# Optimization experiments

Measured on AMD Instinct MI355X. Metric: run time of the kernel, lower is better.

The kernel has to match this reference:

```python
import jax, jax.numpy as jnp
import numpy as np

NUM_BINS = 10
BIN_DISP = 0.5
MIN_REG = 1e-5
H = 22
W = 22
S = 16
C = 256
F_ = H * W


def _distance_map(center, sz):
    # DiMP DistanceMap: soft-binned radial distance from center. [bins, sz0, sz1]
    bins = jnp.arange(NUM_BINS, dtype=jnp.float32)[:, None, None]
    k0 = jnp.arange(sz[0], dtype=jnp.float32)[:, None]
    k1 = jnp.arange(sz[1], dtype=jnp.float32)[None, :]
    dist = jnp.sqrt((k0 - center[0]) ** 2 + (k1 - center[1]) ** 2)
    bd = dist[None] / BIN_DISP - bins
    lower = jax.nn.relu(1.0 - jnp.abs(bd[:-1]))
    last = jnp.clip(1.0 + bd[-1:], 0.0, 1.0)
    return jnp.concatenate([lower, last], axis=0)


def _unfold_map(fm, h, w):
    # Equivalent of F.unfold(full_map,(h,w)).view(h,w,h,w).flip((2,3)).permute(2,3,0,1):
    # out[f=(li,lj), ki, kj] = fm[h-1-li+ki, w-1-lj+kj]
    r = (h - 1 - jnp.arange(h))[:, None] + jnp.arange(h)[None, :]  # [li, ki]
    c = (w - 1 - jnp.arange(w))[:, None] + jnp.arange(w)[None, :]  # [lj, kj]
    m = fm[r[:, None, :, None], c[None, :, None, :]]  # [li, lj, ki, kj]
    return m.reshape(h * w, h, w)


def setup_inputs() -> dict:
    key = jax.random.key(0)
    k1, k2 = jax.random.split(key)
    filt = jax.random.normal(k1, (S, F_, C, 1, 1), jnp.float32) * 0.1
    feat = jax.random.normal(k2, (1, S, C, H, W), jnp.float32)
    d = jnp.arange(NUM_BINS, dtype=jnp.float32) * BIN_DISP
    init_gauss = jnp.exp(-0.5 * d ** 2)  # init_gauss_sigma = 1.0
    return {
        "filt": filt,
        "feat": feat,
        "log_step_length": jnp.zeros((1,), jnp.float32),          # log(1.0)
        "filter_reg": 0.01 * jnp.ones((1,), jnp.float32),
        "label_w": init_gauss - init_gauss.min(),                  # label_map_predictor weights
        "mask_w": 4.0 * jnp.tanh(2.0 - d),                         # target_mask_predictor weights
        "spatial_w": jnp.ones((NUM_BINS,), jnp.float32),           # spatial_weight_predictor weights
        "num_iter": 3,
    }


def _forward(filt, feat, log_step_length, filter_reg, label_w, mask_w, spatial_w, num_iter):
    f2 = feat[0]            # [S, C, H, W]
    w = filt[..., 0, 0]     # [S, F, C]   (1x1 DiCor filters)
    h, wd = feat.shape[-2], feat.shape[-1]
    s, fnum = w.shape[0], w.shape[1]
    sz = (2 * h - 1, 2 * wd - 1)
    center = jnp.array([sz[0] // 2, sz[1] // 2], dtype=jnp.float32)
    dmap = _distance_map(center, sz)  # [bins, 2H-1, 2W-1]
    # 1x1 convs over the bin dimension, then unfold into per-filter maps [F, H, W]
    label_map = _unfold_map(jnp.einsum('bhw,b->hw', dmap, label_w), h, wd)
    target_mask = _unfold_map(jax.nn.sigmoid(jnp.einsum('bhw,b->hw', dmap, mask_w)), h, wd)
    spatial_weight = _unfold_map(jnp.einsum('bhw,b->hw', dmap, spatial_w), h, wd)
    step_length = jnp.exp(log_step_length[0])
    reg_weight = jnp.maximum(filter_reg[0] * filter_reg[0], MIN_REG ** 2)
    a = target_mask
    sw2 = spatial_weight * spatial_weight
    for _ in range(num_iter):
        # apply_filter with 1x1 filters: scores[s,f,h,w] = sum_c feat[s,c,h,w] * w[s,f,c]
        scores = jnp.einsum('schw,sfc->sfhw', f2, w)
        # LeakyReluPar / LeakyReluParDeriv with per-location slope a
        scores_act = 0.5 * (1.0 - a) * jnp.abs(scores) + 0.5 * (1.0 + a) * scores
        score_mask = 0.5 * (1.0 - a) * jnp.sign(scores) + 0.5 * (1.0 + a)
        residuals = score_mask * (sw2 * (scores_act - label_map))
        # apply_feat_transpose with 1x1 filters
        w_grad = jnp.einsum('sfhw,schw->sfc', residuals, f2) + reg_weight * w
        scores_grad = jnp.einsum('schw,sfc->sfhw', f2, w_grad)
        scores_grad = spatial_weight * (score_mask * scores_grad)
        alpha_num = jnp.sum(w_grad * w_grad, axis=2)  # [S, F]
        alpha_den = jnp.maximum(
            jnp.sum((scores_grad * scores_grad).reshape(s, fnum, -1), axis=2)
            + reg_weight * alpha_num, 1e-8)
        alpha = alpha_num / alpha_den
        w = w - step_length * alpha[..., None] * w_grad
    return w[..., None, None]  # [S, F, C, 1, 1]


def reference(filt, feat, log_step_length, filter_reg, label_w, mask_w, spatial_w, num_iter):
    return _forward(filt, feat, log_step_length, filter_reg, label_w, mask_w, spatial_w, num_iter)
```

## Files before the change

kernel.cpp:

```cpp
#include <hip/hip_runtime.h>
#include <math.h>
#include <stdint.h>

#define Ww 22
#define P_ 484
#define S_ 16
#define C_ 256
#define TSZ 1849

typedef _Float16 f16x8 __attribute__((ext_vector_type(8)));
typedef _Float16 f16x4 __attribute__((ext_vector_type(4)));
typedef float f32x4 __attribute__((ext_vector_type(4)));

__device__ __forceinline__ int xcd_chunk(int bid, int chunk) {
    return (bid & 7) * chunk + (bid >> 3);
}

__device__ __forceinline__ void gld16(const _Float16* g, _Float16* lds) {
    auto* lp = (__attribute__((address_space(3))) uint32_t*)(uintptr_t)(lds);
    auto* gp = (const __attribute__((address_space(1))) uint32_t*)(uintptr_t)(g);
    __builtin_amdgcn_global_load_lds(gp, lp, 16, 0, 0);
}

__device__ __forceinline__ f32x4 map_entry(const float* label_w, const float* mask_w,
                                           const float* spatial_w, float d) {
    float lab = 0.f, msk = 0.f, spw = 0.f;
#pragma unroll
    for (int b = 0; b < 9; ++b) {
        float wb = fmaxf(0.f, 1.f - fabsf(d - (float)b));
        lab += wb * label_w[b];
        msk += wb * mask_w[b];
        spw += wb * spatial_w[b];
    }
    float w9 = fminf(fmaxf(1.f + (d - 9.f), 0.f), 1.f);
    lab += w9 * label_w[9];
    msk += w9 * mask_w[9];
    spw += w9 * spatial_w[9];
    f32x4 o;
    o[0] = lab;
    o[1] = 1.f / (1.f + expf(-msk));
    o[2] = spw * spw;
    o[3] = spw;
    return o;
}

__global__ __launch_bounds__(256) void k_pro(
    const float* __restrict__ filt, const float* __restrict__ feat,
    const float* __restrict__ lw, const float* __restrict__ mw,
    const float* __restrict__ sw,
    float* __restrict__ Wf, _Float16* __restrict__ Wh,
    float* __restrict__ num0, float* __restrict__ den0,
    _Float16* __restrict__ f2h, _Float16* __restrict__ f2th,
    f32x4* __restrict__ map4t) {
    int wgid = xcd_chunk(blockIdx.x, 514);
    int x = wgid / 514;
    int local = wgid % 514;
    int t = threadIdx.x;
    if (local == 0) {
        int idx = x + 8 * t;
        if (idx < TSZ) {
            int dx = idx / 43 - 21, dy = idx % 43 - 21;
            float d = sqrtf((float)(dx * dx + dy * dy)) * 2.0f;
            map4t[idx] = map_entry(lw, mw, sw, d);
        }
    } else if (local < 257) {
        int u = local - 1;
        int s = x * 2 + (u >> 7);
        int f = (u & 127) * 4 + (t >> 6);
        int c = (t & 63) * 4;
        size_t oh = ((size_t)(s * 512 + f)) * C_ + c;
        if (f < P_) {
            size_t o = ((size_t)(s * P_ + f)) * C_ + c;
            f32x4 v = *(const f32x4*)(filt + o);
            *(f32x4*)(Wf + o) = v;
            f16x4 h;
#pragma unroll
            for (int q = 0; q < 4; ++q) h[q] = (_Float16)v[q];
            *(f16x4*)(Wh + oh) = h;
            if ((t & 63) == 0) { num0[s * P_ + f] = 0.f; den0[s * P_ + f] = 0.f; }
        } else {
            f16x4 h = {};
            *(f16x4*)(Wh + oh) = h;
        }
    } else if (local < 513) {
        int u = local - 257;
        int s = x * 2 + (u >> 7);
        int rem = u & 127;
        int p0 = (rem & 15) * 32, c0 = (rem >> 4) * 32;
        int cc = t & 31, rr = t >> 5;
        __shared__ float tb[32][33];
#pragma unroll
        for (int q = 0; q < 4; ++q) {
            int c = c0 + rr + q * 8;
            int p = p0 + cc;
            float v = (p < P_) ? feat[((size_t)s * C_ + c) * P_ + p] : 0.f;
            f2h[((size_t)s * C_ + c) * 512 + p] = (_Float16)v;
            tb[rr + q * 8][cc] = v;
        }
        __syncthreads();
#pragma unroll
        for (int q = 0; q < 4; ++q) {
            int p = p0 + rr + q * 8;
            f2th[((size_t)s * 512 + p) * C_ + c0 + cc] = (_Float16)tb[cc][rr + q * 8];
        }
    }
}

template <int EPI, int BM, int KK, int LDA, int LDB, int TPS, int NBN, bool WSG = false>
__global__ __launch_bounds__(256, 4) void k_gemm(
    const _Float16* __restrict__ Ah, const _Float16* __restrict__ Bh,
    const f32x4* __restrict__ map4t, const _Float16* __restrict__ sch_i,
    const _Float16* __restrict__ Wh_i, const float* __restrict__ freg,
    _Float16* __restrict__ out_h, _Float16* __restrict__ out_h3,
    float* __restrict__ red) {
    constexpr int TI = BM / 32, TJ = 2, NT = KK / 128, NIA = BM / 16;
    int tid = threadIdx.x;
    int w = tid >> 6, l = tid & 63;
    int wgid = xcd_chunk(blockIdx.x, S_ * TPS / 8);
    int s = wgid / TPS;
    int rem = wgid % TPS;
    int m0 = (rem / NBN) * BM, n0 = (rem % NBN) * 64;
    int wm = w >> 1, wn = w & 1;
    int r16 = l & 15;

    __shared__ _Float16 As[BM * 128];
    __shared__ _Float16 Bs[64 * 128];

    int lrow = w * 4 + (l >> 4);
    int gsrc = ((l & 15) ^ lrow) << 3;
    const _Float16* gA = Ah + (size_t)s * (512 * LDA) + (size_t)(m0 + lrow) * LDA + gsrc;
    const _Float16* gB = Bh + (size_t)s * 131072 + (size_t)(n0 + lrow) * LDB + gsrc;

    f32x4 acc[TI][TJ] = {};

#pragma unroll
    for (int t = 0; t < NT; ++t) {
#pragma unroll
        for (int i = 0; i < NIA; ++i)
            gld16(gA + (size_t)i * 16 * LDA + t * 128, &As[(i * 16 + w * 4) * 128]);
#pragma unroll
        for (int i = 0; i < 4; ++i)
            gld16(gB + (size_t)i * 16 * LDB + t * 128, &Bs[(i * 16 + w * 4) * 128]);
        __syncthreads();
#pragma unroll
        for (int kk = 0; kk < 4; ++kk) {
            int px = ((kk * 4 + (l >> 4)) ^ r16) << 3;
            f16x8 af[TI], bf[TJ];
#pragma unroll
            for (int ti = 0; ti < TI; ++ti)
                af[ti] = *(const f16x8*)&As[(wm * (BM / 2) + ti * 16 + r16) * 128 + px];
#pragma unroll
            for (int tj = 0; tj < TJ; ++tj)
                bf[tj] = *(const f16x8*)&Bs[(wn * 32 + tj * 16 + r16) * 128 + px];
#pragma unroll
            for (int ti = 0; ti < TI; ++ti)
#pragma unroll
                for (int tj = 0; tj < TJ; ++tj)
                    acc[ti][tj] = __builtin_amdgcn_mfma_f32_16x16x32_f16(
                        af[ti], bf[tj], acc[ti][tj], 0, 0, 0);
        }
        if (t + 1 < NT) __syncthreads();
    }

    int q4 = (l >> 4) * 4;

    if constexpr (EPI == 1) {
#pragma unroll
        for (int ti = 0; ti < TI; ++ti)
#pragma unroll
            for (int r = 0; r < 4; ++r) {
                int m = m0 + wm * (BM / 2) + ti * 16 + q4 + r;
                int im = m / 22, jm = m - im * 22;
#pragma unroll
                for (int tj = 0; tj < TJ; ++tj) {
                    int n = n0 + wn * 32 + tj * 16 + r16;
                    float sc = acc[ti][tj][r];
                    float res = 0.f;
                    size_t po = ((size_t)(s * 512 + m)) * 512 + n;
                    if (m < P_ && n < P_) {
                        int kn = n / 22, ln = n - kn * 22;
                        f32x4 m4 = map4t[(kn - im + 21) * 43 + (ln - jm + 21)];
                        float sgn = (sc > 0.f) ? 1.f : ((sc < 0.f) ? -1.f : 0.f);
                        float msk = 0.5f * (1.f - m4[1]) * sgn + 0.5f * (1.f + m4[1]);
                        res = msk * (m4[2] * (msk * sc - m4[0]));
                    }
                    out_h[po] = (_Float16)res;
                    out_h3[po] = (_Float16)sc;
                }
            }
    } else if constexpr (EPI == 2) {
        float fr = freg[0];
        float regw = fmaxf(fr * fr, 1e-10f);
#pragma unroll
        for (int ti = 0; ti < TI; ++ti)
#pragma unroll
            for (int r = 0; r < 4; ++r) {
                int m = m0 + wm * (BM / 2) + ti * 16 + q4 + r;
                float v = 0.f;
#pragma unroll
                for (int tj = 0; tj < TJ; ++tj) {
                    int n = n0 + wn * 32 + tj * 16 + r16;
                    size_t o = ((size_t)(s * 512 + m)) * C_ + n;
                    float wg = acc[ti][tj][r] + regw * (float)Wh_i[o];
                    out_h[o] = (_Float16)wg;
                    v += wg * wg;
                }
                v += __shfl_xor(v, 1);
                v += __shfl_xor(v, 2);
                v += __shfl_xor(v, 4);
                v += __shfl_xor(v, 8);
                if (r16 == 0 && m < P_) atomicAdd(&red[s * P_ + m], v);
            }
    } else {
#pragma unroll
        for (int ti = 0; ti < TI; ++ti)
#pragma unroll
            for (int r = 0; r < 4; ++r) {
                int m = m0 + wm * (BM / 2) + ti * 16 + q4 + r;
                int im = m / 22, jm = m - im * 22;
                float v = 0.f;
#pragma unroll
                for (int tj = 0; tj < TJ; ++tj) {
                    int n = n0 + wn * 32 + tj * 16 + r16;
                    float a = acc[ti][tj][r];
                    size_t po = ((size_t)(s * 512 + m)) * 512 + n;
                    if constexpr (WSG) out_h[po] = (_Float16)a;
                    if (m < P_ && n < P_) {
                        int kn = n / 22, ln = n - kn * 22;
                        f32x4 m4 = map4t[(kn - im + 21) * 43 + (ln - jm + 21)];
                        float sc = (float)sch_i[po];
                        float sgn = (sc > 0.f) ? 1.f : ((sc < 0.f) ? -1.f : 0.f);
                        float msk = 0.5f * (1.f - m4[1]) * sgn + 0.5f * (1.f + m4[1]);
                        float sg = m4[3] * msk * a;
                        v += sg * sg;
                    }
                }
                v += __shfl_xor(v, 1);
                v += __shfl_xor(v, 2);
                v += __shfl_xor(v, 4);
                v += __shfl_xor(v, 8);
                if (r16 == 0 && m < P_) atomicAdd(&red[s * P_ + m], v);
            }
    }
}

__global__ __launch_bounds__(256) void k_fu(
    float* __restrict__ Wf, _Float16* __restrict__ Wh,
    const _Float16* __restrict__ wgradh,
    const float* __restrict__ num_rd, const float* __restrict__ den_rd,
    float* __restrict__ num_zw, float* __restrict__ den_zw,
    const _Float16* __restrict__ sgrawh, _Float16* __restrict__ scoresh,
    _Float16* __restrict__ residh,
    const f32x4* __restrict__ map4t,
    const float* __restrict__ freg, const float* __restrict__ lsl) {
    int wgid = xcd_chunk(blockIdx.x, 484);
    int s = wgid / 242;
    int local = wgid % 242;
    int t = threadIdx.x;
    float fr = freg[0];
    float regw = fmaxf(fr * fr, 1e-10f);
    float step = expf(lsl[0]);
    if (local < 121) {
        int f = local * 4 + (t >> 6);
        int row = s * P_ + f;
        float nu = num_rd[row], de = den_rd[row];
        float sa = step * (nu / fmaxf(de + regw * nu, 1e-8f));
        int c = (t & 63) * 4;
        size_t o = (size_t)row * C_ + c;
        size_t oh = ((size_t)(s * 512 + f)) * C_ + c;
        f32x4 wv = *(const f32x4*)(Wf + o);
        f16x4 g = *(const f16x4*)(wgradh + oh);
        f16x4 h;
#pragma unroll
        for (int q = 0; q < 4; ++q) {
            wv[q] -= sa * (float)g[q];
            h[q] = (_Float16)wv[q];
        }
        *(f32x4*)(Wf + o) = wv;
        *(f16x4*)(Wh + oh) = h;
        if ((t & 63) == 0) { num_zw[row] = 0.f; den_zw[row] = 0.f; }
    } else {
        int m = (local - 121) * 4 + (t >> 6);
        int row = s * P_ + m;
        float nu = num_rd[row], de = den_rd[row];
        float sa = step * (nu / fmaxf(de + regw * nu, 1e-8f));
        int im = m / 22, jm = m - im * 22;
        int n0 = (t & 63) * 8;
        size_t ro = ((size_t)(s * 512 + m)) * 512 + n0;
        f16x8 so = *(const f16x8*)(scoresh + ro);
        f16x8 gg = *(const f16x8*)(sgrawh + ro);
        f16x8 sn, rs;
#pragma unroll
        for (int j = 0; j < 8; ++j) {
            float sc = (float)so[j] - sa * (float)gg[j];
            sn[j] = (_Float16)sc;
            int n = n0 + j;
            float res = 0.f;
            if (n < P_) {
                int kn = n / 22, ln = n - kn * 22;
                f32x4 m4 = map4t[(kn - im + 21) * 43 + (ln - jm + 21)];
                float sgn = (sc > 0.f) ? 1.f : ((sc < 0.f) ? -1.f : 0.f);
                float msk = 0.5f * (1.f - m4[1]) * sgn + 0.5f * (1.f + m4[1]);
                res = msk * (m4[2] * (msk * sc - m4[0]));
            }
            rs[j] = (_Float16)res;
        }
        *(f16x8*)(scoresh + ro) = sn;
        *(f16x8*)(residh + ro) = rs;
    }
}

__global__ __launch_bounds__(256) void k_update(float* __restrict__ Wf,
                                                const _Float16* __restrict__ wgradh,
                                                const float* __restrict__ num,
                                                const float* __restrict__ den,
                                                const float* __restrict__ freg,
                                                const float* __restrict__ lsl) {
    int wgid = xcd_chunk(blockIdx.x, 242);
    int s = wgid / 121;
    int t = threadIdx.x;
    int f = (wgid % 121) * 4 + (t >> 6);
    int row = s * P_ + f;
    float nu = num[row], de = den[row];
    float fr = freg[0];
    float regw = fmaxf(fr * fr, 1e-10f);
    float sa = expf(lsl[0]) * (nu / fmaxf(de + regw * nu, 1e-8f));
    int c = (t & 63) * 4;
    size_t o = (size_t)row * C_ + c;
    size_t oh = ((size_t)(s * 512 + f)) * C_ + c;
    f32x4 wv = *(const f32x4*)(Wf + o);
    f16x4 g = *(const f16x4*)(wgradh + oh);
#pragma unroll
    for (int q = 0; q < 4; ++q) wv[q] -= sa * (float)g[q];
    *(f32x4*)(Wf + o) = wv;
}

extern "C" void kernel_launch(void* const* d_in, const int* in_sizes, int n_in,
                              void* d_out, int out_size, void* d_ws, size_t ws_size,
                              hipStream_t stream) {
    const float* filt = (const float*)d_in[0];
    const float* feat = (const float*)d_in[1];
    const float* lsl  = (const float*)d_in[2];
    const float* freg = (const float*)d_in[3];
    const float* lw   = (const float*)d_in[4];
    const float* mw   = (const float*)d_in[5];
    const float* sw   = (const float*)d_in[6];
    float* Wf = (float*)d_out;

    char* ws = (char*)d_ws;
    f32x4* map4t     = (f32x4*)ws;      ws += (size_t)TSZ * 16;
    _Float16* residh = (_Float16*)ws;   ws += (size_t)S_ * 512 * 512 * 2;
    _Float16* scoresh= (_Float16*)ws;   ws += (size_t)S_ * 512 * 512 * 2;
    _Float16* sgrawh = (_Float16*)ws;   ws += (size_t)S_ * 512 * 512 * 2;
    _Float16* wgradh = (_Float16*)ws;   ws += (size_t)S_ * 512 * C_ * 2;
    _Float16* Wh     = (_Float16*)ws;   ws += (size_t)S_ * 512 * C_ * 2;
    _Float16* f2h    = (_Float16*)ws;   ws += (size_t)S_ * C_ * 512 * 2;
    _Float16* f2th   = (_Float16*)ws;   ws += (size_t)S_ * 512 * C_ * 2;
    float* num0      = (float*)ws;      ws += (size_t)S_ * P_ * 4;
    float* den0      = (float*)ws;      ws += (size_t)S_ * P_ * 4;
    float* num1      = (float*)ws;      ws += (size_t)S_ * P_ * 4;
    float* den1      = (float*)ws;      ws += (size_t)S_ * P_ * 4;

    k_pro<<<4112, 256, 0, stream>>>(filt, feat, lw, mw, sw, Wf, Wh, num0, den0,
                                    f2h, f2th, map4t);

    k_gemm<1, 64, 256, 256, 256, 64, 8><<<1024, 256, 0, stream>>>(
        Wh, f2th, map4t, nullptr, nullptr, nullptr, residh, scoresh, nullptr);
    k_gemm<2, 32, 512, 512, 512, 64, 4><<<1024, 256, 0, stream>>>(
        residh, f2h, map4t, nullptr, Wh, freg, wgradh, nullptr, num0);
    k_gemm<3, 64, 256, 256, 256, 64, 8, true><<<1024, 256, 0, stream>>>(
        wgradh, f2th, map4t, scoresh, nullptr, nullptr, sgrawh, nullptr, den0);
    k_fu<<<3872, 256, 0, stream>>>(Wf, Wh, wgradh, num0, den0, num1, den1,
                                   sgrawh, scoresh, residh, map4t, freg, lsl);
    k_gemm<2, 32, 512, 512, 512, 64, 4><<<1024, 256, 0, stream>>>(
        residh, f2h, map4t, nullptr, Wh, freg, wgradh, nullptr, num1);
    k_gemm<3, 64, 256, 256, 256, 64, 8, true><<<1024, 256, 0, stream>>>(
        wgradh, f2th, map4t, scoresh, nullptr, nullptr, sgrawh, nullptr, den1);
    k_fu<<<3872, 256, 0, stream>>>(Wf, Wh, wgradh, num1, den1, num0, den0,
                                   sgrawh, scoresh, residh, map4t, freg, lsl);
    k_gemm<2, 32, 512, 512, 512, 64, 4><<<1024, 256, 0, stream>>>(
        residh, f2h, map4t, nullptr, Wh, freg, wgradh, nullptr, num0);
    k_gemm<3, 64, 256, 256, 256, 64, 8, false><<<1024, 256, 0, stream>>>(
        wgradh, f2th, map4t, scoresh, nullptr, nullptr, nullptr, nullptr, den0);
    k_update<<<1936, 256, 0, stream>>>(Wf, wgradh, num0, den0, freg, lsl);
}
```

Before: 128.5 us.

## Fuse filter/score update elementwise pass into the residual-by-features gemm

Replaces the separate elementwise update kernel and the following wgrad gemm with one kernel. It computes the updated scores and residuals on the fly into LDS as the A operand, multiplies them by the features, and then applies the filter step and regularisation in the epilogue. Scores are ping-ponged between two buffers, and six zeroed num/den accumulators are set up once in the prologue so later kernels no longer re-zero them. This removes a kernel launch and the residual round-trip through global memory per iteration. In exchange the residual and score math is recomputed in each of the four N-tile blocks, and the tile is small (32x64, K staged in 128-wide chunks without double buffering).

```diff
diff --git a/kernel.cpp b/kernel.cpp
--- a/kernel.cpp
+++ b/kernel.cpp
@@ -7,6 +7,7 @@
 #define S_ 16
 #define C_ 256
 #define TSZ 1849
+#define NB 7744
 
 typedef _Float16 f16x8 __attribute__((ext_vector_type(8)));
 typedef _Float16 f16x4 __attribute__((ext_vector_type(4)));
@@ -49,7 +50,7 @@
     const float* __restrict__ lw, const float* __restrict__ mw,
     const float* __restrict__ sw,
     float* __restrict__ Wf, _Float16* __restrict__ Wh,
-    float* __restrict__ num0, float* __restrict__ den0,
+    float* __restrict__ nb,
     _Float16* __restrict__ f2h, _Float16* __restrict__ f2th,
     f32x4* __restrict__ map4t) {
     int wgid = xcd_chunk(blockIdx.x, 514);
@@ -77,7 +78,11 @@
 #pragma unroll
             for (int q = 0; q < 4; ++q) h[q] = (_Float16)v[q];
             *(f16x4*)(Wh + oh) = h;
-            if ((t & 63) == 0) { num0[s * P_ + f] = 0.f; den0[s * P_ + f] = 0.f; }
+            if ((t & 63) == 0) {
+                int row = s * P_ + f;
+#pragma unroll
+                for (int b = 0; b < 6; ++b) nb[b * NB + row] = 0.f;
+            }
         } else {
             f16x4 h = {};
             *(f16x4*)(Wh + oh) = h;
@@ -244,69 +249,132 @@
     }
 }
 
-__global__ __launch_bounds__(256) void k_fu(
+__global__ __launch_bounds__(256, 4) void k_g2f(
+    const _Float16* __restrict__ sch_old, _Float16* __restrict__ sch_new,
+    const _Float16* __restrict__ sgrawh, const _Float16* __restrict__ Bh,
     float* __restrict__ Wf, _Float16* __restrict__ Wh,
-    const _Float16* __restrict__ wgradh,
+    _Float16* __restrict__ wgradh,
     const float* __restrict__ num_rd, const float* __restrict__ den_rd,
-    float* __restrict__ num_zw, float* __restrict__ den_zw,
-    const _Float16* __restrict__ sgrawh, _Float16* __restrict__ scoresh,
-    _Float16* __restrict__ residh,
+    float* __restrict__ num_wr,
     const f32x4* __restrict__ map4t,
     const float* __restrict__ freg, const float* __restrict__ lsl) {
-    int wgid = xcd_chunk(blockIdx.x, 484);
-    int s = wgid / 242;
-    int local = wgid % 242;
-    int t = threadIdx.x;
+    __shared__ _Float16 As[32 * 128];
+    __shared__ _Float16 Bs[64 * 128];
+    __shared__ float alpha_l[32];
+
+    int tid = threadIdx.x;
+    int w = tid >> 6, l = tid & 63;
+    int wgid = xcd_chunk(blockIdx.x, 128);
+    int s = wgid / 64;
+    int rem = wgid % 64;
+    int m0 = (rem >> 2) * 32, n0 = (rem & 3) * 64;
+    int wm = w >> 1, wn = w & 1;
+    int r16 = l & 15;
+
     float fr = freg[0];
     float regw = fmaxf(fr * fr, 1e-10f);
     float step = expf(lsl[0]);
-    if (local < 121) {
-        int f = local * 4 + (t >> 6);
-        int row = s * P_ + f;
-        float nu = num_rd[row], de = den_rd[row];
-        float sa = step * (nu / fmaxf(de + regw * nu, 1e-8f));
-        int c = (t & 63) * 4;
-        size_t o = (size_t)row * C_ + c;
-        size_t oh = ((size_t)(s * 512 + f)) * C_ + c;
-        f32x4 wv = *(const f32x4*)(Wf + o);
-        f16x4 g = *(const f16x4*)(wgradh + oh);
-        f16x4 h;
-#pragma unroll
-        for (int q = 0; q < 4; ++q) {
-            wv[q] -= sa * (float)g[q];
-            h[q] = (_Float16)wv[q];
-        }
-        *(f32x4*)(Wf + o) = wv;
-        *(f16x4*)(Wh + oh) = h;
-        if ((t & 63) == 0) { num_zw[row] = 0.f; den_zw[row] = 0.f; }
-    } else {
-        int m = (local - 121) * 4 + (t >> 6);
-        int row = s * P_ + m;
-        float nu = num_rd[row], de = den_rd[row];
-        float sa = step * (nu / fmaxf(de + regw * nu, 1e-8f));
-        int im = m / 22, jm = m - im * 22;
-        int n0 = (t & 63) * 8;
-        size_t ro = ((size_t)(s * 512 + m)) * 512 + n0;
-        f16x8 so = *(const f16x8*)(scoresh + ro);
-        f16x8 gg = *(const f16x8*)(sgrawh + ro);
-        f16x8 sn, rs;
-#pragma unroll
-        for (int j = 0; j < 8; ++j) {
-            float sc = (float)so[j] - sa * (float)gg[j];
-            sn[j] = (_Float16)sc;
-            int n = n0 + j;
-            float res = 0.f;
-            if (n < P_) {
-                int kn = n / 22, ln = n - kn * 22;
-                f32x4 m4 = map4t[(kn - im + 21) * 43 + (ln - jm + 21)];
-                float sgn = (sc > 0.f) ? 1.f : ((sc < 0.f) ? -1.f : 0.f);
-                float msk = 0.5f * (1.f - m4[1]) * sgn + 0.5f * (1.f + m4[1]);
-                res = msk * (m4[2] * (msk * sc - m4[0]));
-            }
-            rs[j] = (_Float16)res;
-        }
-        *(f16x8*)(scoresh + ro) = sn;
-        *(f16x8*)(residh + ro) = rs;
+
+    if (tid < 32) {
+        int mg = m0 + tid;
+        float a = 0.f;
+        if (mg < P_) {
+            int row = s * P_ + mg;
+            float nu = num_rd[row], de = den_rd[row];
+            a = step * (nu / fmaxf(de + regw * nu, 1e-8f));
+        }
+        alpha_l[tid] = a;
+    }
+    __syncthreads();
+
+    int lrow = w * 4 + (l >> 4);
+    int gsrc = ((l & 15) ^ lrow) << 3;
+    const _Float16* gB = Bh + (size_t)s * 131072 + (size_t)(n0 + lrow) * 512 + gsrc;
+
+    f32x4 acc[2] = {};
+    bool wr_sc = (n0 == 0);
+    size_t sbase = ((size_t)(s * 512 + m0)) * 512;
+
+#pragma unroll
+    for (int t = 0; t < 4; ++t) {
+#pragma unroll
+        for (int i = 0; i < 4; ++i)
+            gld16(gB + (size_t)i * 16 * 512 + t * 128, &Bs[(i * 16 + w * 4) * 128]);
+#pragma unroll
+        for (int i = 0; i < 2; ++i) {
+            int gidx = tid + i * 256;
+            int row = gidx >> 4, g = gidx & 15;
+            int mg = m0 + row;
+            int im = mg / 22, jm = mg - im * 22;
+            size_t ro = sbase + (size_t)row * 512 + t * 128 + g * 8;
+            f16x8 so = *(const f16x8*)(sch_old + ro);
+            f16x8 sg = *(const f16x8*)(sgrawh + ro);
+            float sa = alpha_l[row];
+            f16x8 sn, rs;
+#pragma unroll
+            for (int j = 0; j < 8; ++j) {
+                float sc = (float)so[j] - sa * (float)sg[j];
+                sn[j] = (_Float16)sc;
+                int n = t * 128 + g * 8 + j;
+                float res = 0.f;
+                if (mg < P_ && n < P_) {
+                    int kn = n / 22, ln = n - kn * 22;
+                    f32x4 m4 = map4t[(kn - im + 21) * 43 + (ln - jm + 21)];
+                    float sgn = (sc > 0.f) ? 1.f : ((sc < 0.f) ? -1.f : 0.f);
+                    float msk = 0.5f * (1.f - m4[1]) * sgn + 0.5f * (1.f + m4[1]);
+                    res = msk * (m4[2] * (msk * sc - m4[0]));
+                }
+                rs[j] = (_Float16)res;
+            }
+            *(f16x8*)&As[row * 128 + ((g ^ (row & 15)) << 3)] = rs;
+            if (wr_sc) *(f16x8*)(sch_new + ro) = sn;
+        }
+        __syncthreads();
+#pragma unroll
+        for (int kk = 0; kk < 4; ++kk) {
+            int px = ((kk * 4 + (l >> 4)) ^ r16) << 3;
+            f16x8 af = *(const f16x8*)&As[(wm * 16 + r16) * 128 + px];
+            f16x8 bf[2];
+#pragma unroll
+            for (int tj = 0; tj < 2; ++tj)
+                bf[tj] = *(const f16x8*)&Bs[(wn * 32 + tj * 16 + r16) * 128 + px];
+#pragma unroll
+            for (int tj = 0; tj < 2; ++tj)
+                acc[tj] = __builtin_amdgcn_mfma_f32_16x16x32_f16(af, bf[tj], acc[tj], 0, 0, 0);
+        }
+        if (t + 1 < 4) __syncthreads();
+    }
+
+    int q4 = (l >> 4) * 4;
+#pragma unroll
+    for (int r = 0; r < 4; ++r) {
+        int m_l = wm * 16 + q4 + r;
+        int m = m0 + m_l;
+        float sa = alpha_l[m_l];
+        float v = 0.f;
+#pragma unroll
+        for (int tj = 0; tj < 2; ++tj) {
+            int c = n0 + wn * 32 + tj * 16 + r16;
+            size_t oh = ((size_t)(s * 512 + m)) * C_ + c;
+            float a = acc[tj][r];
+            float wg;
+            if (m < P_) {
+                size_t o = ((size_t)(s * P_ + m)) * C_ + c;
+                float wf = Wf[o] - sa * (float)wgradh[oh];
+                Wf[o] = wf;
+                Wh[oh] = (_Float16)wf;
+                wg = a + regw * wf;
+            } else {
+                wg = a;
+            }
+            wgradh[oh] = (_Float16)wg;
+            v += wg * wg;
+        }
+        v += __shfl_xor(v, 1);
+        v += __shfl_xor(v, 2);
+        v += __shfl_xor(v, 4);
+        v += __shfl_xor(v, 8);
+        if (r16 == 0 && m < P_) atomicAdd(&num_wr[s * P_ + m], v);
     }
 }
 
@@ -350,37 +418,34 @@
     char* ws = (char*)d_ws;
     f32x4* map4t     = (f32x4*)ws;      ws += (size_t)TSZ * 16;
     _Float16* residh = (_Float16*)ws;   ws += (size_t)S_ * 512 * 512 * 2;
-    _Float16* scoresh= (_Float16*)ws;   ws += (size_t)S_ * 512 * 512 * 2;
+    _Float16* sc0    = (_Float16*)ws;   ws += (size_t)S_ * 512 * 512 * 2;
+    _Float16* sc1    = (_Float16*)ws;   ws += (size_t)S_ * 512 * 512 * 2;
     _Float16* sgrawh = (_Float16*)ws;   ws += (size_t)S_ * 512 * 512 * 2;
     _Float16* wgradh = (_Float16*)ws;   ws += (size_t)S_ * 512 * C_ * 2;
     _Float16* Wh     = (_Float16*)ws;   ws += (size_t)S_ * 512 * C_ * 2;
     _Float16* f2h    = (_Float16*)ws;   ws += (size_t)S_ * C_ * 512 * 2;
     _Float16* f2th   = (_Float16*)ws;   ws += (size_t)S_ * 512 * C_ * 2;
-    float* num0      = (float*)ws;      ws += (size_t)S_ * P_ * 4;
-    float* den0      = (float*)ws;      ws += (size_t)S_ * P_ * 4;
-    float* num1      = (float*)ws;      ws += (size_t)S_ * P_ * 4;
-    float* den1      = (float*)ws;      ws += (size_t)S_ * P_ * 4;
-
-    k_pro<<<4112, 256, 0, stream>>>(filt, feat, lw, mw, sw, Wf, Wh, num0, den0,
+    float* nb        = (float*)ws;      ws += (size_t)6 * NB * 4;
+    float* num0 = nb,          * den0 = nb + NB;
+    float* num1 = nb + 2 * NB, * den1 = nb + 3 * NB;
+    float* num2 = nb + 4 * NB, * den2 = nb + 5 * NB;
+
+    k_pro<<<4112, 256, 0, stream>>>(filt, feat, lw, mw, sw, Wf, Wh, nb,
                                     f2h, f2th, map4t);
 
     k_gemm<1, 64, 256, 256, 256, 64, 8><<<1024, 256, 0, stream>>>(
-        Wh, f2th, map4t, nullptr, nullptr, nullptr, residh, scoresh, nullptr);
+        Wh, f2th, map4t, nullptr, nullptr, nullptr, residh, sc0, nullptr);
     k_gemm<2, 32, 512, 512, 512, 64, 4><<<1024, 256, 0, stream>>>(
         residh, f2h, map4t, nullptr, Wh, freg, wgradh, nullptr, num0);
     k_gemm<3, 64, 256, 256, 256, 64, 8, true><<<1024, 256, 0, stream>>>(
-        wgradh, f2th, map4t, scoresh, nullptr, nullptr, sgrawh, nullptr, den0);
-    k_fu<<<3872, 256, 0, stream>>>(Wf, Wh, wgradh, num0, den0, num1, den1,
-                                   sgrawh, scoresh, residh, map4t, freg, lsl);
-    k_gemm<2, 32, 512, 512, 512, 64, 4><<<1024, 256, 0, stream>>>(
-        residh, f2h, map4t, nullptr, Wh, freg, wgradh, nullptr, num1);
+        wgradh, f2th, map4t, sc0, nullptr, nullptr, sgrawh, nullptr, den0);
+    k_g2f<<<1024, 256, 0, stream>>>(sc0, sc1, sgrawh, f2h, Wf, Wh, wgradh,
+                                    num0, den0, num1, map4t, freg, lsl);
     k_gemm<3, 64, 256, 256, 256, 64, 8, true><<<1024, 256, 0, stream>>>(
-        wgradh, f2th, map4t, scoresh, nullptr, nullptr, sgrawh, nullptr, den1);
-    k_fu<<<3872, 256, 0, stream>>>(Wf, Wh, wgradh, num1, den1, num0, den0,
-                                   sgrawh, scoresh, residh, map4t, freg, lsl);
-    k_gemm<2, 32, 512, 512, 512, 64, 4><<<1024, 256, 0, stream>>>(
-        residh, f2h, map4t, nullptr, Wh, freg, wgradh, nullptr, num0);
+        wgradh, f2th, map4t, sc1, nullptr, nullptr, sgrawh, nullptr, den1);
+    k_g2f<<<1024, 256, 0, stream>>>(sc1, sc0, sgrawh, f2h, Wf, Wh, wgradh,
+                                    num1, den1, num2, map4t, freg, lsl);
     k_gemm<3, 64, 256, 256, 256, 64, 8, false><<<1024, 256, 0, stream>>>(
-        wgradh, f2th, map4t, scoresh, nullptr, nullptr, nullptr, nullptr, den0);
-    k_update<<<1936, 256, 0, stream>>>(Wf, wgradh, num0, den0, freg, lsl);
-}
+        wgradh, f2th, map4t, sc0, nullptr, nullptr, nullptr, nullptr, den2);
+    k_update<<<1936, 256, 0, stream>>>(Wf, wgradh, num2, den2, freg, lsl);
+}
```

Result: slower. 148.1 us (+15.2%).
